# Performance work log

Hardware: AMD Instinct MI355X
Metric: run time of the kernel (lower is better)

Reference implementation:

```python
import jax, jax.numpy as jnp
import numpy as np

B, C, H, W = 2, 256, 80, 160
G, P, E = 8, 8, 2  # groups(heads), sampling points, ffn expansion
LN_EPS = 1e-5


def setup_inputs() -> dict:
    key = jax.random.key(0)
    ks = jax.random.split(key, 12)
    def n(k, shape, s=1.0):
        return jax.random.normal(k, shape, dtype=jnp.float32) * s
    return dict(
        feats=n(ks[0], (B, C, H, W)),
        feats_pos=n(ks[1], (B, C, H, W)),
        anchor_points=jax.random.uniform(ks[2], (B, H, W, 2), dtype=jnp.float32),
        value_W=n(ks[3], (C, C), 0.02), value_b=jnp.zeros((C,), jnp.float32),
        off_W=n(ks[4], (C, G * P * 2), 0.02), off_b=n(ks[5], (G * P * 2,), 0.02),
        attn_W=n(ks[6], (C, G * P), 0.02), attn_b=jnp.zeros((G * P,), jnp.float32),
        out_W=n(ks[7], (C, C), 0.02), out_b=jnp.zeros((C,), jnp.float32),
        ln1_g=jnp.ones((C,), jnp.float32), ln1_b=jnp.zeros((C,), jnp.float32),
        ln2_g=jnp.ones((C,), jnp.float32), ln2_b=jnp.zeros((C,), jnp.float32),
        ffn_w1=n(ks[8], (E * C, C), 0.02), ffn_b1=jnp.zeros((E * C,), jnp.float32),
        ffn_w2=n(ks[9], (C, E * C), 0.02), ffn_b2=jnp.zeros((C,), jnp.float32),
    )


def _layernorm(x, g, b):
    m = jnp.mean(x, axis=-1, keepdims=True)
    v = jnp.mean(jnp.square(x - m), axis=-1, keepdims=True)
    return (x - m) * jax.lax.rsqrt(v + LN_EPS) * g + b


def _bilinear_sample(value, px, py, h, w):
    # value: [b,G,HW,cg]; px,py: [b,G,P,HW] pixel coords (align_corners=False)
    x0 = jnp.floor(px); y0 = jnp.floor(py)
    wx1 = px - x0; wx0 = 1.0 - wx1
    wy1 = py - y0; wy0 = 1.0 - wy1
    vexp = value[:, :, None, :, :]  # [b,G,1,HW,cg]
    def gather(xi, yi):
        valid = ((xi >= 0) & (xi < w) & (yi >= 0) & (yi < h)).astype(value.dtype)
        xc = jnp.clip(xi, 0, w - 1).astype(jnp.int32)
        yc = jnp.clip(yi, 0, h - 1).astype(jnp.int32)
        idx = yc * w + xc  # [b,G,P,HW]
        v = jnp.take_along_axis(vexp, idx[..., None], axis=3)  # [b,G,P,HW,cg]
        return v * valid[..., None]
    return (gather(x0, y0) * (wx0 * wy0)[..., None]
            + gather(x0 + 1, y0) * (wx1 * wy0)[..., None]
            + gather(x0, y0 + 1) * (wx0 * wy1)[..., None]
            + gather(x0 + 1, y0 + 1) * (wx1 * wy1)[..., None])


def reference(feats, feats_pos, anchor_points,
              value_W, value_b, off_W, off_b, attn_W, attn_b, out_W, out_b,
              ln1_g, ln1_b, ln2_g, ln2_b, ffn_w1, ffn_b1, ffn_w2, ffn_b2):
    b, c, h, w = feats.shape
    hw = h * w
    cg = c // G
    x = feats + feats_pos                              # residual input (pos-encoded)
    q = x.reshape(b, c, hw).transpose(0, 2, 1)         # [b,HW,c]
    # deformable attention
    val = (q @ value_W + value_b).reshape(b, hw, G, cg).transpose(0, 2, 1, 3)   # [b,G,HW,cg]
    off = (q @ off_W + off_b).reshape(b, hw, G, P, 2).transpose(0, 2, 3, 1, 4)  # [b,G,P,HW,2]
    attn = jax.nn.softmax((q @ attn_W + attn_b).reshape(b, hw, G, P)
                          .transpose(0, 2, 3, 1), axis=2)                        # [b,G,P,HW]
    anchor = anchor_points.reshape(b, hw, 2)[:, None, None, :, :]               # [b,1,1,HW,2]
    loc = anchor + off / jnp.array([w, h], dtype=off.dtype)                     # normalized xy
    px = loc[..., 0] * w - 0.5
    py = loc[..., 1] * h - 0.5
    sampled = _bilinear_sample(val, px, py, h, w)                               # [b,G,P,HW,cg]
    agg = jnp.einsum('bgpn,bgpnc->bngc', attn, sampled).reshape(b, hw, c)
    upd = agg @ out_W + out_b
    # residual + LN1
    y = _layernorm(q + upd, ln1_g, ln1_b)
    # conv1x1 - SiLU - conv1x1 FFN + residual + LN2
    ffn = jax.nn.silu(y @ ffn_w1.T + ffn_b1) @ ffn_w2.T + ffn_b2
    y = _layernorm(y + ffn, ln2_g, ln2_b)
    return y.transpose(0, 2, 1).reshape(b, c, h, w)
```

## Files before the change

### kernel.cpp

```cpp
#include <hip/hip_runtime.h>
#include <hip/hip_bf16.h>
#include <math.h>
#include <stdint.h>

#define B_ 2
#define C_ 256
#define H_ 80
#define W_ 160
#define HW_ (H_*W_)
#define NTOK (B_*HW_)
#define G_ 8
#define P_ 8
#define NQKV 448
#define NQKVP 512

typedef __bf16 bf16;
typedef __attribute__((ext_vector_type(8))) __bf16 bf16x8;
typedef __attribute__((ext_vector_type(4))) float f32x4;

__device__ __forceinline__ void gload_lds16(const void* g, void* l) {
  __builtin_amdgcn_global_load_lds(
      (__attribute__((address_space(1))) void*)g,
      (__attribute__((address_space(3))) void*)l,
      16, 0, 0);
}

__global__ __launch_bounds__(256)
void prep_weights(const float* __restrict__ vW, const float* __restrict__ vb,
                  const float* __restrict__ oW, const float* __restrict__ ob,
                  const float* __restrict__ aW, const float* __restrict__ ab,
                  const float* __restrict__ outW,
                  const float* __restrict__ w1, const float* __restrict__ w2,
                  bf16* __restrict__ wqkv, float* __restrict__ bqkv,
                  bf16* __restrict__ woutt, bf16* __restrict__ w1b, bf16* __restrict__ w2b)
{
  int i = blockIdx.x * 256 + threadIdx.x;
  if (i < NQKVP*256) {
    int nn = i >> 8, k = i & 255;
    float w;
    if (nn < 256)      w = vW[k*256 + nn];
    else if (nn < 384) w = oW[k*128 + (nn-256)];
    else if (nn < 448) w = aW[k*64  + (nn-384)];
    else               w = 0.f;
    wqkv[i] = (bf16)w;
  }
  int j = i - NQKVP*256;
  if (j >= 0 && j < 256*256) {
    int nn = j >> 8, k = j & 255;
    woutt[j] = (bf16)outW[k*256 + nn];
  }
  int j2 = i - (NQKVP*256 + 256*256);
  if (j2 >= 0 && j2 < 512*256) w1b[j2] = (bf16)w1[j2];
  int j3 = i - (NQKVP*256 + 256*256 + 512*256);
  if (j3 >= 0 && j3 < 256*512) w2b[j3] = (bf16)w2[j3];
  int j4 = i - (NQKVP*256 + 256*256 + 512*256 + 256*512);
  if (j4 >= 0 && j4 < NQKVP) {
    float bv;
    if (j4 < 256)      bv = vb[j4];
    else if (j4 < 384) bv = ob[j4-256];
    else if (j4 < 448) bv = ab[j4-384];
    else               bv = 0.f;
    bqkv[j4] = bv;
  }
}

__global__ __launch_bounds__(256)
void qprep_kernel(const float* __restrict__ f, const float* __restrict__ fp,
                  bf16* __restrict__ qb)
{
  __shared__ float lt[64][65];
  const int tid = threadIdx.x;
  const int n0 = blockIdx.x * 64;
  const int c0 = blockIdx.y * 64;
  const int b  = blockIdx.z;
#pragma unroll
  for (int i = 0; i < 16; ++i) {
    int cl = i*4 + (tid >> 6), nl = tid & 63;
    size_t gi = ((size_t)(b*C_ + c0 + cl))*HW_ + n0 + nl;
    lt[cl][nl] = f[gi] + fp[gi];
  }
  __syncthreads();
#pragma unroll
  for (int i = 0; i < 16; ++i) {
    int nl = i*4 + (tid >> 6), cl = tid & 63;
    size_t qi = ((size_t)(b*HW_ + n0 + nl))*C_ + c0 + cl;
    qb[qi] = (bf16)lt[cl][nl];
  }
}

template<int EPI, int KTOT>
__global__ __launch_bounds__(256)
void gemm_kernel(const bf16* __restrict__ A, const bf16* __restrict__ Bt,
                 const float* __restrict__ bias,
                 void* __restrict__ out0, float* __restrict__ out1,
                 float* __restrict__ out2)
{
  __shared__ bf16 lA[128*64];
  __shared__ bf16 lB[128*64];
  const int tid  = threadIdx.x;
  const int wave = tid >> 6, lane = tid & 63;
  const int m0 = blockIdx.x * 128, n0 = blockIdx.y * 128;
  const int wm = wave >> 1, wn = wave & 1;
  const int fr = lane & 15;
  const int fq = lane >> 4;
  f32x4 acc[4][4] = {};

  for (int kc = 0; kc < KTOT/64; ++kc) {
    if (kc) __syncthreads();
#pragma unroll
    for (int it = 0; it < 4; ++it) {
      int chunk = it*256 + tid;
      int row = chunk >> 3, cb = chunk & 7;
      int ksw = ((cb ^ (row & 7)) << 3);
      gload_lds16(A  + (size_t)(m0+row)*KTOT + kc*64 + ksw,
                  (char*)lA + it*4096 + wave*1024);
      gload_lds16(Bt + (size_t)(n0+row)*KTOT + kc*64 + ksw,
                  (char*)lB + it*4096 + wave*1024);
    }
    __syncthreads();
#pragma unroll
    for (int ks = 0; ks < 2; ++ks) {
      bf16x8 af[4], bg[4];
#pragma unroll
      for (int i = 0; i < 4; ++i) {
        int ar = wm*64 + i*16 + fr;
        af[i] = *(const bf16x8*)&lA[ar*64 + (((ks*4 + fq) ^ (ar & 7)) << 3)];
        int br = wn*64 + i*16 + fr;
        bg[i] = *(const bf16x8*)&lB[br*64 + (((ks*4 + fq) ^ (br & 7)) << 3)];
      }
#pragma unroll
      for (int mi = 0; mi < 4; ++mi)
#pragma unroll
        for (int ni = 0; ni < 4; ++ni)
          acc[mi][ni] = __builtin_amdgcn_mfma_f32_16x16x32_bf16(af[mi], bg[ni], acc[mi][ni], 0, 0, 0);
    }
  }

#pragma unroll
  for (int mi = 0; mi < 4; ++mi)
#pragma unroll
  for (int ni = 0; ni < 4; ++ni)
#pragma unroll
  for (int r = 0; r < 4; ++r) {
    int row = m0 + wm*64 + mi*16 + fq*4 + r;
    int col = n0 + wn*64 + ni*16 + fr;
    float v = acc[mi][ni][r] + bias[col];
    if (EPI == 0) {
      if (col < 256) {
        int g = col >> 5, ch = col & 31;
        int b = row >= HW_ ? 1 : 0;
        int n = row - b*HW_;
        ((bf16*)out0)[(((size_t)(b*G_ + g))*HW_ + n)*32 + ch] = (bf16)v;
      }
      else if (col < 384) out1[(size_t)row*128 + (col-256)] = v;
      else if (col < 448) out2[(size_t)row*64  + (col-384)] = v;
    } else {
      float s = v / (1.0f + __expf(-v));
      ((bf16*)out0)[(size_t)row*512 + col] = (bf16)s;
    }
  }
}

template<int KTOT, bool NCHW_OUT>
__global__ __launch_bounds__(512)
void gemm_ln64_kernel(const bf16* __restrict__ A, const bf16* __restrict__ Bt,
                      const float* __restrict__ bias, const bf16* __restrict__ res,
                      const float* __restrict__ gg, const float* __restrict__ bb,
                      bf16* __restrict__ yb, float* __restrict__ outf)
{
  __shared__ __align__(16) char smem[40960];
  bf16* lA = (bf16*)smem;
  bf16* lB = (bf16*)(smem + 8192);
  float (*lt)[68] = (float(*)[68])smem;
  __shared__ float2 red[64][4];
  const int tid  = threadIdx.x;
  const int wave = tid >> 6, lane = tid & 63;
  const int m0 = blockIdx.x * 64;
  const int wm = wave >> 2, wn = wave & 3;
  const int fr = lane & 15;
  const int fq = lane >> 4;
  f32x4 acc[2][4] = {};

  for (int kc = 0; kc < KTOT/64; ++kc) {
    if (kc) __syncthreads();
    {
      int row = tid >> 3, cb = tid & 7;
      gload_lds16(A + (size_t)(m0+row)*KTOT + kc*64 + ((cb ^ (row&7))<<3),
                  (char*)lA + wave*1024);
    }
#pragma unroll
    for (int it = 0; it < 4; ++it) {
      int chunk = it*512 + tid;
      int row = chunk >> 3, cb = chunk & 7;
      gload_lds16(Bt + (size_t)row*KTOT + kc*64 + ((cb ^ (row&7))<<3),
                  (char*)lB + it*8192 + wave*1024);
    }
    __syncthreads();
#pragma unroll
    for (int ks = 0; ks < 2; ++ks) {
      bf16x8 af[2], bg[4];
#pragma unroll
      for (int i = 0; i < 2; ++i) {
        int ar = wm*32 + i*16 + fr;
        af[i] = *(const bf16x8*)&lA[ar*64 + (((ks*4 + fq) ^ (ar&7))<<3)];
      }
#pragma unroll
      for (int i = 0; i < 4; ++i) {
        int br = wn*64 + i*16 + fr;
        bg[i] = *(const bf16x8*)&lB[br*64 + (((ks*4 + fq) ^ (br&7))<<3)];
      }
#pragma unroll
      for (int mi = 0; mi < 2; ++mi)
#pragma unroll
        for (int ni = 0; ni < 4; ++ni)
          acc[mi][ni] = __builtin_amdgcn_mfma_f32_16x16x32_bf16(af[mi], bg[ni], acc[mi][ni], 0, 0, 0);
    }
  }

  float gcol[4], bcol[4];
#pragma unroll
  for (int ni = 0; ni < 4; ++ni) {
    int col = wn*64 + ni*16 + fr;
    gcol[ni] = gg[col]; bcol[ni] = bb[col];
  }
#pragma unroll
  for (int mi = 0; mi < 2; ++mi)
#pragma unroll
  for (int r = 0; r < 4; ++r) {
    int rowl = wm*32 + mi*16 + fq*4 + r;
    size_t rowg = (size_t)(m0 + rowl);
    float s = 0.f, q = 0.f;
#pragma unroll
    for (int ni = 0; ni < 4; ++ni) {
      int col = wn*64 + ni*16 + fr;
      float v = acc[mi][ni][r] + bias[col] + (float)res[rowg*256 + col];
      acc[mi][ni][r] = v;
      s += v; q += v*v;
    }
#pragma unroll
    for (int o = 1; o < 16; o <<= 1) { s += __shfl_xor(s, o, 64); q += __shfl_xor(q, o, 64); }
    if (fr == 0) red[rowl][wn] = make_float2(s, q);
  }
  __syncthreads();
#pragma unroll
  for (int mi = 0; mi < 2; ++mi)
#pragma unroll
  for (int r = 0; r < 4; ++r) {
    int rowl = wm*32 + mi*16 + fq*4 + r;
    float s = 0.f, q = 0.f;
#pragma unroll
    for (int k = 0; k < 4; ++k) { float2 p = red[rowl][k]; s += p.x; q += p.y; }
    const float mean = s * (1.f/256.f);
    const float var  = q * (1.f/256.f) - mean*mean;
    const float rs   = rsqrtf(var + 1e-5f);
#pragma unroll
    for (int ni = 0; ni < 4; ++ni)
      acc[mi][ni][r] = (acc[mi][ni][r] - mean)*rs*gcol[ni] + bcol[ni];
  }

  if constexpr (!NCHW_OUT) {
#pragma unroll
    for (int mi = 0; mi < 2; ++mi)
#pragma unroll
    for (int ni = 0; ni < 4; ++ni)
#pragma unroll
    for (int r = 0; r < 4; ++r) {
      size_t rowg = (size_t)(m0 + wm*32 + mi*16 + fq*4 + r);
      int col = wn*64 + ni*16 + fr;
      yb[rowg*256 + col] = (bf16)acc[mi][ni][r];
    }
  } else {
    const int bq = m0 / HW_;
    const int n0 = m0 % HW_;
    __syncthreads();
#pragma unroll
    for (int ch = 0; ch < 4; ++ch) {
      if (ch) __syncthreads();
      if (wn == ch) {
#pragma unroll
        for (int mi = 0; mi < 2; ++mi)
#pragma unroll
        for (int ni = 0; ni < 4; ++ni)
#pragma unroll
        for (int r = 0; r < 4; ++r)
          lt[ni*16 + fr][wm*32 + mi*16 + fq*4 + r] = acc[mi][ni][r];
      }
      __syncthreads();
#pragma unroll
      for (int j = 0; j < 2; ++j) {
        int flat = j*512 + tid;
        int cl = flat >> 4, t4 = (flat & 15) * 4;
        float4 v4 = *(const float4*)&lt[cl][t4];
        *(float4*)&outf[((size_t)(bq*C_ + ch*64 + cl))*HW_ + n0 + t4] = v4;
      }
    }
  }
}

__global__ __launch_bounds__(256)
void sample_kernel(const bf16* __restrict__ val, const float* __restrict__ off,
                   const float* __restrict__ attnl, const float* __restrict__ anchors,
                   bf16* __restrict__ agg)
{
  const int tid  = threadIdx.x;
  const int lane = tid & 63;
  const int wv   = tid >> 6;
  const int c8   = lane & 3;
  const int bid  = blockIdx.x;
  const int g    = bid & 7;
  const int chunk= bid >> 3;
  const int t    = chunk*64 + wv*16 + (lane >> 2);
  const int b    = (t >= HW_) ? 1 : 0;

  const float2 anc = *(const float2*)(anchors + (size_t)t*2);
  const float ax = anc.x * W_ - 0.5f;
  const float ay = anc.y * H_ - 0.5f;

  const float4 l0 = *(const float4*)(attnl + (size_t)t*64 + g*8);
  const float4 l1 = *(const float4*)(attnl + (size_t)t*64 + g*8 + 4);
  float l[8] = {l0.x, l0.y, l0.z, l0.w, l1.x, l1.y, l1.z, l1.w};
  float mx = l[0];
#pragma unroll
  for (int p = 1; p < 8; ++p) mx = fmaxf(mx, l[p]);
  float s = 0.f;
#pragma unroll
  for (int p = 0; p < 8; ++p) { l[p] = __expf(l[p] - mx); s += l[p]; }
  const float inv = 1.f / s;

  const float4* opv = (const float4*)(off + (size_t)t*128 + g*16);
  const float4 o0 = opv[0], o1 = opv[1], o2 = opv[2], o3 = opv[3];
  const float ox[8] = {o0.x, o0.z, o1.x, o1.z, o2.x, o2.z, o3.x, o3.z};
  const float oy[8] = {o0.y, o0.w, o1.y, o1.w, o2.y, o2.w, o3.y, o3.w};

  const bf16* vb = val + ((size_t)(b*G_ + g)*HW_)*32 + c8*8;

  float a[8] = {};
#pragma unroll
  for (int p = 0; p < 8; ++p) {
    const float px = ax + ox[p], py = ay + oy[p];
    const float x0f = floorf(px), y0f = floorf(py);
    const int x0 = (int)x0f, y0 = (int)y0f;
    const float wx1 = px - x0f, wx0 = 1.f - wx1;
    const float wy1 = py - y0f, wy0 = 1.f - wy1;
    const float ap = l[p] * inv;
    float w00 = ap*wx0*wy0, w10 = ap*wx1*wy0, w01 = ap*wx0*wy1, w11 = ap*wx1*wy1;
    const bool vx0 = (unsigned)x0 < W_, vx1 = (unsigned)(x0+1) < W_;
    const bool vy0 = (unsigned)y0 < H_, vy1 = (unsigned)(y0+1) < H_;
    w00 = (vx0 && vy0) ? w00 : 0.f;  w10 = (vx1 && vy0) ? w10 : 0.f;
    w01 = (vx0 && vy1) ? w01 : 0.f;  w11 = (vx1 && vy1) ? w11 : 0.f;
    const int xc0 = min(max(x0, 0), W_-1),   xc1 = min(max(x0+1, 0), W_-1);
    const int yc0 = min(max(y0, 0), H_-1),   yc1 = min(max(y0+1, 0), H_-1);
    const bf16x8 v00 = *(const bf16x8*)(vb + (size_t)(yc0*W_ + xc0)*32);
    const bf16x8 v10 = *(const bf16x8*)(vb + (size_t)(yc0*W_ + xc1)*32);
    const bf16x8 v01 = *(const bf16x8*)(vb + (size_t)(yc1*W_ + xc0)*32);
    const bf16x8 v11 = *(const bf16x8*)(vb + (size_t)(yc1*W_ + xc1)*32);
#pragma unroll
    for (int c = 0; c < 8; ++c)
      a[c] += w00*(float)v00[c] + w10*(float)v10[c]
            + w01*(float)v01[c] + w11*(float)v11[c];
  }
  bf16 r[8];
#pragma unroll
  for (int c = 0; c < 8; ++c) r[c] = (bf16)a[c];
  *(bf16x8*)(agg + (size_t)t*256 + g*32 + c8*8) = *(bf16x8*)r;
}

extern "C" void kernel_launch(void* const* d_in, const int* in_sizes, int n_in,
                              void* d_out, int out_size, void* d_ws, size_t ws_size,
                              hipStream_t stream)
{
  const float* feats   = (const float*)d_in[0];
  const float* featsp  = (const float*)d_in[1];
  const float* anchors = (const float*)d_in[2];
  const float* value_W = (const float*)d_in[3];
  const float* value_b = (const float*)d_in[4];
  const float* off_W   = (const float*)d_in[5];
  const float* off_b   = (const float*)d_in[6];
  const float* attn_W  = (const float*)d_in[7];
  const float* attn_b  = (const float*)d_in[8];
  const float* out_W   = (const float*)d_in[9];
  const float* out_b   = (const float*)d_in[10];
  const float* ln1_g   = (const float*)d_in[11];
  const float* ln1_b   = (const float*)d_in[12];
  const float* ln2_g   = (const float*)d_in[13];
  const float* ln2_b   = (const float*)d_in[14];
  const float* w1      = (const float*)d_in[15];
  const float* b1      = (const float*)d_in[16];
  const float* w2      = (const float*)d_in[17];
  const float* b2      = (const float*)d_in[18];
  float* out = (float*)d_out;

  char* ws = (char*)d_ws;
  size_t cur = 0;
  auto alloc = [&](size_t bytes) -> char* {
    char* p = ws + cur;
    cur += (bytes + 255) & ~(size_t)255;
    return p;
  };
  bf16*  wqkv  = (bf16*) alloc((size_t)NQKVP*256*2);
  bf16*  woutt = (bf16*) alloc((size_t)256*256*2);
  bf16*  w1b   = (bf16*) alloc((size_t)512*256*2);
  bf16*  w2b   = (bf16*) alloc((size_t)256*512*2);
  float* bqkv  = (float*)alloc((size_t)NQKVP*4);
  bf16*  qb    = (bf16*) alloc((size_t)NTOK*256*2);
  bf16*  valb  = (bf16*) alloc((size_t)NTOK*256*2);
  float* offv  = (float*)alloc((size_t)NTOK*128*4);
  float* attnl = (float*)alloc((size_t)NTOK*64*4);
  bf16*  aggb  = (bf16*) alloc((size_t)NTOK*256*2);
  bf16*  y1b   = (bf16*) alloc((size_t)NTOK*256*2);
  bf16*  hb    = (bf16*) alloc((size_t)NTOK*512*2);

  prep_weights<<<(NQKVP*256 + 256*256 + 512*256 + 256*512 + NQKVP + 255)/256, 256, 0, stream>>>(
      value_W, value_b, off_W, off_b, attn_W, attn_b, out_W, w1, w2,
      wqkv, bqkv, woutt, w1b, w2b);

  qprep_kernel<<<dim3(HW_/64, C_/64, B_), 256, 0, stream>>>(feats, featsp, qb);

  gemm_kernel<0, 256><<<dim3(NTOK/128, NQKVP/128), 256, 0, stream>>>(
      qb, wqkv, bqkv, valb, offv, attnl);

  sample_kernel<<<NTOK/8, 256, 0, stream>>>(valb, offv, attnl, anchors, aggb);

  gemm_ln64_kernel<256, false><<<NTOK/64, 512, 0, stream>>>(
      aggb, woutt, out_b, qb, ln1_g, ln1_b, y1b, nullptr);

  gemm_kernel<2, 256><<<dim3(NTOK/128, 512/128), 256, 0, stream>>>(
      y1b, w1b, b1, hb, nullptr, nullptr);

  gemm_ln64_kernel<512, true><<<NTOK/64, 512, 0, stream>>>(
      hb, w2b, b2, y1b, ln2_g, ln2_b, nullptr, out);
}
```

Baseline: 133.1 us.

## Merge weight prep and q-prep launches; batch bilinear gathers per four points

Merges the weight conversion kernel and the feats+pos transpose kernel into a single launch, with blocks picking their job from the block index, which saves one launch and the gap between the two. In the sampling kernel, the point loop is split into two batches of four points. Each batch computes all weights and offsets first, then issues all sixteen gathers before accumulating, so more memory loads are in flight at once. This raises register pressure in the sample kernel, which may reduce occupancy.

```diff
diff --git a/kernel.cpp b/kernel.cpp
--- a/kernel.cpp
+++ b/kernel.cpp
@@ -13,6 +13,7 @@
 #define P_ 8
 #define NQKV 448
 #define NQKVP 512
+#define PREP_BLOCKS 1794
 
 typedef __bf16 bf16;
 typedef __attribute__((ext_vector_type(8))) __bf16 bf16x8;
@@ -26,65 +27,66 @@
 }
 
 __global__ __launch_bounds__(256)
-void prep_weights(const float* __restrict__ vW, const float* __restrict__ vb,
-                  const float* __restrict__ oW, const float* __restrict__ ob,
-                  const float* __restrict__ aW, const float* __restrict__ ab,
-                  const float* __restrict__ outW,
-                  const float* __restrict__ w1, const float* __restrict__ w2,
-                  bf16* __restrict__ wqkv, float* __restrict__ bqkv,
-                  bf16* __restrict__ woutt, bf16* __restrict__ w1b, bf16* __restrict__ w2b)
-{
-  int i = blockIdx.x * 256 + threadIdx.x;
-  if (i < NQKVP*256) {
-    int nn = i >> 8, k = i & 255;
-    float w;
-    if (nn < 256)      w = vW[k*256 + nn];
-    else if (nn < 384) w = oW[k*128 + (nn-256)];
-    else if (nn < 448) w = aW[k*64  + (nn-384)];
-    else               w = 0.f;
-    wqkv[i] = (bf16)w;
-  }
-  int j = i - NQKVP*256;
-  if (j >= 0 && j < 256*256) {
-    int nn = j >> 8, k = j & 255;
-    woutt[j] = (bf16)outW[k*256 + nn];
-  }
-  int j2 = i - (NQKVP*256 + 256*256);
-  if (j2 >= 0 && j2 < 512*256) w1b[j2] = (bf16)w1[j2];
-  int j3 = i - (NQKVP*256 + 256*256 + 512*256);
-  if (j3 >= 0 && j3 < 256*512) w2b[j3] = (bf16)w2[j3];
-  int j4 = i - (NQKVP*256 + 256*256 + 512*256 + 256*512);
-  if (j4 >= 0 && j4 < NQKVP) {
-    float bv;
-    if (j4 < 256)      bv = vb[j4];
-    else if (j4 < 384) bv = ob[j4-256];
-    else if (j4 < 448) bv = ab[j4-384];
-    else               bv = 0.f;
-    bqkv[j4] = bv;
-  }
-}
-
-__global__ __launch_bounds__(256)
-void qprep_kernel(const float* __restrict__ f, const float* __restrict__ fp,
-                  bf16* __restrict__ qb)
+void prep_kernel(const float* __restrict__ vW, const float* __restrict__ vb,
+                 const float* __restrict__ oW, const float* __restrict__ ob,
+                 const float* __restrict__ aW, const float* __restrict__ ab,
+                 const float* __restrict__ outW,
+                 const float* __restrict__ w1, const float* __restrict__ w2,
+                 const float* __restrict__ f, const float* __restrict__ fp,
+                 bf16* __restrict__ wqkv, float* __restrict__ bqkv,
+                 bf16* __restrict__ woutt, bf16* __restrict__ w1b,
+                 bf16* __restrict__ w2b, bf16* __restrict__ qb)
 {
   __shared__ float lt[64][65];
   const int tid = threadIdx.x;
-  const int n0 = blockIdx.x * 64;
-  const int c0 = blockIdx.y * 64;
-  const int b  = blockIdx.z;
-#pragma unroll
-  for (int i = 0; i < 16; ++i) {
-    int cl = i*4 + (tid >> 6), nl = tid & 63;
-    size_t gi = ((size_t)(b*C_ + c0 + cl))*HW_ + n0 + nl;
-    lt[cl][nl] = f[gi] + fp[gi];
-  }
-  __syncthreads();
-#pragma unroll
-  for (int i = 0; i < 16; ++i) {
-    int nl = i*4 + (tid >> 6), cl = tid & 63;
-    size_t qi = ((size_t)(b*HW_ + n0 + nl))*C_ + c0 + cl;
-    qb[qi] = (bf16)lt[cl][nl];
+  const int bid = blockIdx.x;
+  if (bid < PREP_BLOCKS) {
+    int i = bid * 256 + tid;
+    if (i < NQKVP*256) {
+      int nn = i >> 8, k = i & 255;
+      float w;
+      if (nn < 256)      w = vW[k*256 + nn];
+      else if (nn < 384) w = oW[k*128 + (nn-256)];
+      else if (nn < 448) w = aW[k*64  + (nn-384)];
+      else               w = 0.f;
+      wqkv[i] = (bf16)w;
+    }
+    int j = i - NQKVP*256;
+    if (j >= 0 && j < 256*256) {
+      int nn = j >> 8, k = j & 255;
+      woutt[j] = (bf16)outW[k*256 + nn];
+    }
+    int j2 = i - (NQKVP*256 + 256*256);
+    if (j2 >= 0 && j2 < 512*256) w1b[j2] = (bf16)w1[j2];
+    int j3 = i - (NQKVP*256 + 256*256 + 512*256);
+    if (j3 >= 0 && j3 < 256*512) w2b[j3] = (bf16)w2[j3];
+    int j4 = i - (NQKVP*256 + 256*256 + 512*256 + 256*512);
+    if (j4 >= 0 && j4 < NQKVP) {
+      float bv;
+      if (j4 < 256)      bv = vb[j4];
+      else if (j4 < 384) bv = ob[j4-256];
+      else if (j4 < 448) bv = ab[j4-384];
+      else               bv = 0.f;
+      bqkv[j4] = bv;
+    }
+  } else {
+    const int b2 = bid - PREP_BLOCKS;
+    const int n0 = (b2 % 200) * 64;
+    const int c0 = ((b2 / 200) & 3) * 64;
+    const int b  = b2 / 800;
+#pragma unroll
+    for (int i = 0; i < 16; ++i) {
+      int cl = i*4 + (tid >> 6), nl = tid & 63;
+      size_t gi = ((size_t)(b*C_ + c0 + cl))*HW_ + n0 + nl;
+      lt[cl][nl] = f[gi] + fp[gi];
+    }
+    __syncthreads();
+#pragma unroll
+    for (int i = 0; i < 16; ++i) {
+      int nl = i*4 + (tid >> 6), cl = tid & 63;
+      size_t qi = ((size_t)(b*HW_ + n0 + nl))*C_ + c0 + cl;
+      qb[qi] = (bf16)lt[cl][nl];
+    }
   }
 }
 
@@ -336,28 +338,44 @@
 
   float a[8] = {};
 #pragma unroll
-  for (int p = 0; p < 8; ++p) {
-    const float px = ax + ox[p], py = ay + oy[p];
-    const float x0f = floorf(px), y0f = floorf(py);
-    const int x0 = (int)x0f, y0 = (int)y0f;
-    const float wx1 = px - x0f, wx0 = 1.f - wx1;
-    const float wy1 = py - y0f, wy0 = 1.f - wy1;
-    const float ap = l[p] * inv;
-    float w00 = ap*wx0*wy0, w10 = ap*wx1*wy0, w01 = ap*wx0*wy1, w11 = ap*wx1*wy1;
-    const bool vx0 = (unsigned)x0 < W_, vx1 = (unsigned)(x0+1) < W_;
-    const bool vy0 = (unsigned)y0 < H_, vy1 = (unsigned)(y0+1) < H_;
-    w00 = (vx0 && vy0) ? w00 : 0.f;  w10 = (vx1 && vy0) ? w10 : 0.f;
-    w01 = (vx0 && vy1) ? w01 : 0.f;  w11 = (vx1 && vy1) ? w11 : 0.f;
-    const int xc0 = min(max(x0, 0), W_-1),   xc1 = min(max(x0+1, 0), W_-1);
-    const int yc0 = min(max(y0, 0), H_-1),   yc1 = min(max(y0+1, 0), H_-1);
-    const bf16x8 v00 = *(const bf16x8*)(vb + (size_t)(yc0*W_ + xc0)*32);
-    const bf16x8 v10 = *(const bf16x8*)(vb + (size_t)(yc0*W_ + xc1)*32);
-    const bf16x8 v01 = *(const bf16x8*)(vb + (size_t)(yc1*W_ + xc0)*32);
-    const bf16x8 v11 = *(const bf16x8*)(vb + (size_t)(yc1*W_ + xc1)*32);
-#pragma unroll
-    for (int c = 0; c < 8; ++c)
-      a[c] += w00*(float)v00[c] + w10*(float)v10[c]
-            + w01*(float)v01[c] + w11*(float)v11[c];
+  for (int pb = 0; pb < 2; ++pb) {
+    float w4[4][4];
+    int   ofs[4][4];
+#pragma unroll
+    for (int pi = 0; pi < 4; ++pi) {
+      const int p = pb*4 + pi;
+      const float px = ax + ox[p], py = ay + oy[p];
+      const float x0f = floorf(px), y0f = floorf(py);
+      const int x0 = (int)x0f, y0 = (int)y0f;
+      const float wx1 = px - x0f, wx0 = 1.f - wx1;
+      const float wy1 = py - y0f, wy0 = 1.f - wy1;
+      const float ap = l[p] * inv;
+      const bool vx0 = (unsigned)x0 < W_, vx1 = (unsigned)(x0+1) < W_;
+      const bool vy0 = (unsigned)y0 < H_, vy1 = (unsigned)(y0+1) < H_;
+      w4[pi][0] = (vx0 && vy0) ? ap*wx0*wy0 : 0.f;
+      w4[pi][1] = (vx1 && vy0) ? ap*wx1*wy0 : 0.f;
+      w4[pi][2] = (vx0 && vy1) ? ap*wx0*wy1 : 0.f;
+      w4[pi][3] = (vx1 && vy1) ? ap*wx1*wy1 : 0.f;
+      const int xc0 = min(max(x0, 0), W_-1),   xc1 = min(max(x0+1, 0), W_-1);
+      const int yc0 = min(max(y0, 0), H_-1),   yc1 = min(max(y0+1, 0), H_-1);
+      ofs[pi][0] = (yc0*W_ + xc0)*32;
+      ofs[pi][1] = (yc0*W_ + xc1)*32;
+      ofs[pi][2] = (yc1*W_ + xc0)*32;
+      ofs[pi][3] = (yc1*W_ + xc1)*32;
+    }
+    bf16x8 v[4][4];
+#pragma unroll
+    for (int pi = 0; pi < 4; ++pi)
+#pragma unroll
+      for (int cn = 0; cn < 4; ++cn)
+        v[pi][cn] = *(const bf16x8*)(vb + ofs[pi][cn]);
+#pragma unroll
+    for (int pi = 0; pi < 4; ++pi)
+#pragma unroll
+      for (int cn = 0; cn < 4; ++cn)
+#pragma unroll
+        for (int c = 0; c < 8; ++c)
+          a[c] += w4[pi][cn] * (float)v[pi][cn][c];
   }
   bf16 r[8];
 #pragma unroll
@@ -410,11 +428,9 @@
   bf16*  y1b   = (bf16*) alloc((size_t)NTOK*256*2);
   bf16*  hb    = (bf16*) alloc((size_t)NTOK*512*2);
 
-  prep_weights<<<(NQKVP*256 + 256*256 + 512*256 + 256*512 + NQKVP + 255)/256, 256, 0, stream>>>(
+  prep_kernel<<<PREP_BLOCKS + 1600, 256, 0, stream>>>(
       value_W, value_b, off_W, off_b, attn_W, attn_b, out_W, w1, w2,
-      wqkv, bqkv, woutt, w1b, w2b);
-
-  qprep_kernel<<<dim3(HW_/64, C_/64, B_), 256, 0, stream>>>(feats, featsp, qb);
+      feats, featsp, wqkv, bqkv, woutt, w1b, w2b, qb);
 
   gemm_kernel<0, 256><<<dim3(NTOK/128, NQKVP/128), 256, 0, stream>>>(
       qb, wqkv, bqkv, valb, offv, attnl);
```

Result: no change. 132.1 us (median of 2 runs) (-0.7%).
